# Kernel tuning notes

Measured on AMD Instinct MI355X. Metric: run time of the kernel, lower is better.

The kernel has to match this reference:

```python
import jax, jax.numpy as jnp
import numpy as np

ENC_H = 512      # encoder_hidden_dim -> encoder_out feature = 2*ENC_H
DEC_H = 512      # decoder_hidden_dim
B, S = 32, 2048  # batch, max_seq_len


def setup_inputs() -> dict:
    key = jax.random.key(0)
    k1, k2, k3, k4, k5, k6, k7 = jax.random.split(key, 7)
    encoder_out = jax.random.normal(k1, (B, S, 2 * ENC_H), dtype=jnp.float32)
    hidden = jax.random.normal(k2, (B, DEC_H), dtype=jnp.float32)
    lengths = jax.random.randint(k3, (B,), 1, S + 1, dtype=jnp.int64)
    in_dim = 2 * ENC_H + DEC_H
    # torch nn.Linear default init scale
    attn_w = jax.random.uniform(k4, (DEC_H, in_dim), jnp.float32, -1.0, 1.0) / np.sqrt(in_dim)
    attn_b = jax.random.uniform(k5, (DEC_H,), jnp.float32, -1.0, 1.0) / np.sqrt(in_dim)
    v_w = jax.random.uniform(k6, (1, DEC_H), jnp.float32, -1.0, 1.0) / np.sqrt(DEC_H)
    v_b = jax.random.uniform(k7, (1,), jnp.float32, -1.0, 1.0) / np.sqrt(DEC_H)
    return {"encoder_out": encoder_out, "hidden": hidden, "lengths": lengths,
            "attn_w": attn_w, "attn_b": attn_b, "v_w": v_w, "v_b": v_b}


def reference(encoder_out, hidden, lengths, attn_w, attn_b, v_w, v_b):
    # encoder_out: [B,S,2E], hidden: [B,D], lengths: [B]
    Bc, Sc, _ = encoder_out.shape
    h = jnp.broadcast_to(hidden[:, None, :], (Bc, Sc, hidden.shape[-1]))
    temp = jnp.concatenate([h, encoder_out], axis=2)           # [B,S,D+2E]
    e = jnp.tanh(jnp.einsum('bsf,df->bsd', temp, attn_w) + attn_b)  # [B,S,D]
    scores = jnp.einsum('bsd,d->bs', e, v_w[0]) + v_b[0]       # [B,S]
    mask = jnp.arange(Sc)[None, :] < lengths[:, None]          # [B,S]
    scores = jnp.where(mask, scores, -jnp.inf)
    energy = jax.nn.softmax(scores, axis=1)                    # softmax over valid positions
    energy = jnp.where(mask, energy, 0.0)                      # padded positions stay exactly 0
    context = jnp.einsum('bs,bse->be', energy, encoder_out)    # [B,2E]
    return context
```

## Files before the change

### kernel.cpp

```cpp
#include <hip/hip_runtime.h>
#include <hip/hip_bf16.h>
#include <math.h>

typedef __attribute__((ext_vector_type(4))) short short4v;
typedef __attribute__((ext_vector_type(8))) short short8;
typedef __attribute__((ext_vector_type(16))) float f32x16;

static constexpr int B  = 32;
static constexpr int S  = 2048;
static constexpr int D  = 512;
static constexpr int KE = 1024;
static constexpr int IN = 1536;

__device__ __forceinline__ unsigned pk2(float lo, float hi) {
    __hip_bfloat162 t = __float22bfloat162_rn(make_float2(lo, hi));
    unsigned u;
    __builtin_memcpy(&u, &t, 4);
    return u;
}

__device__ __forceinline__ short4v pack4(float4 f) {
    unsigned u2[2] = { pk2(f.x, f.y), pk2(f.z, f.w) };
    short4v r;
    __builtin_memcpy(&r, u2, 8);
    return r;
}

__device__ __forceinline__ short8 pack8(float4 f0, float4 f1) {
    unsigned u[4] = { pk2(f0.x, f0.y), pk2(f0.z, f0.w), pk2(f1.x, f1.y), pk2(f1.z, f1.w) };
    short8 r;
    __builtin_memcpy(&r, u, 16);
    return r;
}

__device__ __forceinline__ short8 cat44(short4v lo, short4v hi) {
    short8 r;
    __builtin_memcpy(&r, &lo, 8);
    __builtin_memcpy(((char*)&r) + 8, &hi, 8);
    return r;
}

__device__ __forceinline__ float tanh_fast(float x) {
    float e = __expf(2.0f * x);
    return (e - 1.0f) * __builtin_amdgcn_rcpf(e + 1.0f);
}

__global__ void k_prep(const float* __restrict__ attn_w,
                       const float* __restrict__ hidden,
                       const float* __restrict__ attn_b,
                       unsigned short* __restrict__ Bf,
                       float* __restrict__ u) {
    if (blockIdx.x < 256) {
        int o = blockIdx.x * 256 + threadIdx.x;
        int l6  = o & 63;
        int grp = o >> 6;
        int d = (grp & 15) * 32 + (l6 & 31);
        int k = (grp >> 4) * 16 + (l6 >> 5) * 8;
        const float* src = attn_w + (size_t)d * IN + 512 + k;
        float4 f0 = *(const float4*)src;
        float4 f1 = *(const float4*)(src + 4);
        ((short8*)Bf)[o] = pack8(f0, f1);
    } else {
        int gid = (blockIdx.x - 256) * 256 + threadIdx.x;
        int b = gid >> 9;
        int d = gid & (D - 1);
        const float* h = hidden + b * D;
        const float* w = attn_w + (size_t)d * IN;
        float acc = attn_b[d];
        for (int k = 0; k < D; k += 4) {
            float4 hv = *(const float4*)(h + k);
            float4 wv = *(const float4*)(w + k);
            acc += hv.x * wv.x + hv.y * wv.y + hv.z * wv.z + hv.w * wv.w;
        }
        u[gid] = acc;
    }
}

#define LOADB(K, DST) do {                                     \
    _Pragma("unroll")                                          \
    for (int _jt = 0; _jt < 4; _jt++)                          \
        DST[_jt] = bb[(size_t)(K) * 1024 + _jt * 64];          \
} while (0)

__global__ __launch_bounds__(256, 3) void k_fused(
    const float* __restrict__ enc, const unsigned short* __restrict__ Bfrag,
    const float* __restrict__ u, const float* __restrict__ v_w,
    const float* __restrict__ v_b, const int* __restrict__ lengths,
    float* __restrict__ num, float* __restrict__ den)
{
    __shared__ short4v ldsA[2][32 * 19];
    __shared__ float sPart[4][32];
    __shared__ float sExp[32];

    const int b   = blockIdx.y;
    const int s0  = blockIdx.x * 32;
    const int len = lengths[b];
    if (s0 >= len) return;

    const int tid = threadIdx.x;
    const int w   = tid >> 6;
    const int l   = tid & 63;

    const float* encb = enc + ((size_t)b * S + s0) * KE;
    const int mr = tid >> 4;
    const int cw = tid & 15;
    const float* aG = encb + (size_t)mr * KE + cw * 4;
    const int wbase = mr * 19 + cw;

    const short8* bb = (const short8*)Bfrag + (w * 4) * 64 + l;

    f32x16 acc[4];
    #pragma unroll
    for (int jt = 0; jt < 4; jt++)
        #pragma unroll
        for (int e = 0; e < 16; e++) acc[jt][e] = 0.f;

    short8 pb[2][4];
    LOADB(0, pb[0]);
    LOADB(1, pb[1]);

    {
        float4 g0 = *(const float4*)aG;
        float4 g1 = *(const float4*)(aG + (size_t)16 * KE);
        ldsA[0][wbase]           = pack4(g0);
        ldsA[0][wbase + 16 * 19] = pack4(g1);
    }
    __syncthreads();

    const int rb0 = (l & 31) * 19 + (l >> 5) * 2;

    #pragma unroll 1
    for (int c = 0; c < 16; ++c) {
        const int buf = c & 1;
        const int cn  = (c + 1) & 15;
        float4 g0 = *(const float4*)(aG + cn * 64);
        float4 g1 = *(const float4*)(aG + (size_t)16 * KE + cn * 64);
        #pragma unroll
        for (int t2 = 0; t2 < 4; ++t2) {
            const short4v* base = &ldsA[buf][t2 * 4];
            short8 a0 = cat44(base[rb0], base[rb0 + 1]);
            const int bp = t2 & 1;
            #pragma unroll
            for (int jt = 0; jt < 4; jt++)
                acc[jt] = __builtin_amdgcn_mfma_f32_32x32x16_bf16(a0, pb[bp][jt], acc[jt], 0, 0, 0);
            LOADB((c * 4 + t2 + 2) & 63, pb[bp]);
        }
        __syncthreads();
        ldsA[buf ^ 1][wbase]           = pack4(g0);
        ldsA[buf ^ 1][wbase + 16 * 19] = pack4(g1);
        __syncthreads();
    }

    float vv[4], uu[4];
    const float* ub = u + b * D;
    #pragma unroll
    for (int jt = 0; jt < 4; jt++) {
        int d = w * 128 + jt * 32 + (l & 31);
        vv[jt] = v_w[d];
        uu[jt] = ub[d];
    }
    float red[16];
    #pragma unroll
    for (int r = 0; r < 16; r++) {
        float s = 0.f;
        #pragma unroll
        for (int jt = 0; jt < 4; jt++)
            s += vv[jt] * tanh_fast(acc[jt][r] + uu[jt]);
        red[r] = s;
    }
    #pragma unroll
    for (int off = 16; off >= 1; off >>= 1)
        #pragma unroll
        for (int r = 0; r < 16; r++)
            red[r] += __shfl_xor(red[r], off);
    if ((l & 31) == 0) {
        int hb = (l >> 5) * 4;
        #pragma unroll
        for (int r = 0; r < 16; r++)
            sPart[w][(r & 3) + 8 * (r >> 2) + hb] = red[r];
    }
    __syncthreads();

    if (tid < 32) {
        float sc = sPart[0][tid] + sPart[1][tid] + sPart[2][tid] + sPart[3][tid] + v_b[0];
        float wexp = (s0 + tid < len) ? __expf(sc) : 0.f;
        sExp[tid] = wexp;
        float dsum = wexp;
        #pragma unroll
        for (int off = 16; off >= 1; off >>= 1) dsum += __shfl_xor(dsum, off);
        if (tid == 0) atomicAdd(den + b, dsum);
    }
    __syncthreads();

    const float4* e4 = (const float4*)encb;
    float4 cacc[4];
    #pragma unroll
    for (int j = 0; j < 4; j++) cacc[j] = make_float4(0.f, 0.f, 0.f, 0.f);
    #pragma unroll
    for (int i = 0; i < 8; i++) {
        #pragma unroll
        for (int j = 0; j < 4; j++) {
            float wgt = sExp[i * 4 + j];
            float4 v = e4[(size_t)(i * 4 + j) * 256 + tid];
            cacc[j].x += wgt * v.x; cacc[j].y += wgt * v.y;
            cacc[j].z += wgt * v.z; cacc[j].w += wgt * v.w;
        }
    }
    #pragma unroll
    for (int j = 1; j < 4; j++) {
        cacc[0].x += cacc[j].x; cacc[0].y += cacc[j].y;
        cacc[0].z += cacc[j].z; cacc[0].w += cacc[j].w;
    }
    float* o = num + b * KE + tid * 4;
    atomicAdd(o + 0, cacc[0].x);
    atomicAdd(o + 1, cacc[0].y);
    atomicAdd(o + 2, cacc[0].z);
    atomicAdd(o + 3, cacc[0].w);
}

__global__ void k_norm(const float* __restrict__ num, const float* __restrict__ den,
                       float* __restrict__ out) {
    int b = blockIdx.x;
    int t = threadIdx.x;
    float inv = 1.f / den[b];
    float4 v = ((const float4*)(num + b * KE))[t];
    v.x *= inv; v.y *= inv; v.z *= inv; v.w *= inv;
    ((float4*)(out + b * KE))[t] = v;
}

extern "C" void kernel_launch(void* const* d_in, const int* in_sizes, int n_in,
                              void* d_out, int out_size, void* d_ws, size_t ws_size,
                              hipStream_t stream) {
    const float* enc    = (const float*)d_in[0];
    const float* hidden = (const float*)d_in[1];
    const int*   lengths= (const int*)d_in[2];
    const float* attn_w = (const float*)d_in[3];
    const float* attn_b = (const float*)d_in[4];
    const float* v_w    = (const float*)d_in[5];
    const float* v_b    = (const float*)d_in[6];
    float* out = (float*)d_out;

    float* ws  = (float*)d_ws;
    float* u   = ws;
    float* num = u + B * D;
    float* den = num + B * KE;
    unsigned short* Bf = (unsigned short*)(den + 32);

    (void)hipMemsetAsync(num, 0, (size_t)(B * KE + B) * sizeof(float), stream);
    k_prep <<<dim3(320), 256, 0, stream>>>(attn_w, hidden, attn_b, Bf, u);
    k_fused<<<dim3(S / 32, B), 256, 0, stream>>>(enc, Bf, u, v_w, v_b, lengths, num, den);
    k_norm <<<dim3(B), 256, 0, stream>>>(num, den, out);
}
```

Measured before the change: 451.8 us.

## Double M-tile per block to 64 rows, reusing B fragments across two MFMA tiles

Each block now handles 64 sequence positions instead of 32, with two 32-row accumulator sets that share each loaded B fragment, halving B-fragment traffic per row. The A-tile staging loop is restructured to a single sync per chunk, storing the next chunk before computing the current one, with four prefetched float4 loads per thread. Launch bounds drop to 2 blocks/SM to make room for the doubled accumulators. The costs are lower occupancy, coarser masking granularity (more wasted work past the sequence length), and fewer blocks overall.

```diff
diff --git a/kernel.cpp b/kernel.cpp
--- a/kernel.cpp
+++ b/kernel.cpp
@@ -82,18 +82,18 @@
         DST[_jt] = bb[(size_t)(K) * 1024 + _jt * 64];          \
 } while (0)
 
-__global__ __launch_bounds__(256, 3) void k_fused(
+__global__ __launch_bounds__(256, 2) void k_fused(
     const float* __restrict__ enc, const unsigned short* __restrict__ Bfrag,
     const float* __restrict__ u, const float* __restrict__ v_w,
     const float* __restrict__ v_b, const int* __restrict__ lengths,
     float* __restrict__ num, float* __restrict__ den)
 {
-    __shared__ short4v ldsA[2][32 * 19];
-    __shared__ float sPart[4][32];
-    __shared__ float sExp[32];
+    __shared__ short4v ldsA[2][64 * 19];
+    __shared__ float sPart[4][64];
+    __shared__ float sExp[64];
 
     const int b   = blockIdx.y;
-    const int s0  = blockIdx.x * 32;
+    const int s0  = blockIdx.x * 64;
     const int len = lengths[b];
     if (s0 >= len) return;
 
@@ -109,46 +109,54 @@
 
     const short8* bb = (const short8*)Bfrag + (w * 4) * 64 + l;
 
-    f32x16 acc[4];
-    #pragma unroll
-    for (int jt = 0; jt < 4; jt++)
-        #pragma unroll
-        for (int e = 0; e < 16; e++) acc[jt][e] = 0.f;
+    f32x16 acc[2][4];
+    #pragma unroll
+    for (int mt = 0; mt < 2; mt++)
+        #pragma unroll
+        for (int jt = 0; jt < 4; jt++)
+            #pragma unroll
+            for (int e = 0; e < 16; e++) acc[mt][jt][e] = 0.f;
 
     short8 pb[2][4];
     LOADB(0, pb[0]);
     LOADB(1, pb[1]);
 
-    {
-        float4 g0 = *(const float4*)aG;
-        float4 g1 = *(const float4*)(aG + (size_t)16 * KE);
-        ldsA[0][wbase]           = pack4(g0);
-        ldsA[0][wbase + 16 * 19] = pack4(g1);
-    }
-    __syncthreads();
+    float4 g[4];
+    #pragma unroll
+    for (int i = 0; i < 4; i++) g[i] = *(const float4*)(aG + (size_t)i * 16 * KE);
 
     const int rb0 = (l & 31) * 19 + (l >> 5) * 2;
+    const int rb1 = rb0 + 32 * 19;
 
     #pragma unroll 1
-    for (int c = 0; c < 16; ++c) {
-        const int buf = c & 1;
-        const int cn  = (c + 1) & 15;
-        float4 g0 = *(const float4*)(aG + cn * 64);
-        float4 g1 = *(const float4*)(aG + (size_t)16 * KE + cn * 64);
-        #pragma unroll
-        for (int t2 = 0; t2 < 4; ++t2) {
-            const short4v* base = &ldsA[buf][t2 * 4];
-            short8 a0 = cat44(base[rb0], base[rb0 + 1]);
-            const int bp = t2 & 1;
-            #pragma unroll
-            for (int jt = 0; jt < 4; jt++)
-                acc[jt] = __builtin_amdgcn_mfma_f32_32x32x16_bf16(a0, pb[bp][jt], acc[jt], 0, 0, 0);
-            LOADB((c * 4 + t2 + 2) & 63, pb[bp]);
-        }
+    for (int c = 0; c <= 16; ++c) {
         __syncthreads();
-        ldsA[buf ^ 1][wbase]           = pack4(g0);
-        ldsA[buf ^ 1][wbase + 16 * 19] = pack4(g1);
-        __syncthreads();
+        if (c < 16) {
+            #pragma unroll
+            for (int i = 0; i < 4; i++)
+                ldsA[c & 1][wbase + i * 16 * 19] = pack4(g[i]);
+            if (c < 15) {
+                #pragma unroll
+                for (int i = 0; i < 4; i++)
+                    g[i] = *(const float4*)(aG + (size_t)i * 16 * KE + (c + 1) * 64);
+            }
+        }
+        if (c > 0) {
+            const int buf = (c - 1) & 1;
+            #pragma unroll
+            for (int t2 = 0; t2 < 4; ++t2) {
+                const short4v* base = &ldsA[buf][t2 * 4];
+                short8 a0 = cat44(base[rb0], base[rb0 + 1]);
+                short8 a1 = cat44(base[rb1], base[rb1 + 1]);
+                const int bp = t2 & 1;
+                #pragma unroll
+                for (int jt = 0; jt < 4; jt++) {
+                    acc[0][jt] = __builtin_amdgcn_mfma_f32_32x32x16_bf16(a0, pb[bp][jt], acc[0][jt], 0, 0, 0);
+                    acc[1][jt] = __builtin_amdgcn_mfma_f32_32x32x16_bf16(a1, pb[bp][jt], acc[1][jt], 0, 0, 0);
+                }
+                LOADB(((c - 1) * 4 + t2 + 2) & 63, pb[bp]);
+            }
+        }
     }
 
     float vv[4], uu[4];
@@ -159,36 +167,41 @@
         vv[jt] = v_w[d];
         uu[jt] = ub[d];
     }
-    float red[16];
-    #pragma unroll
-    for (int r = 0; r < 16; r++) {
-        float s = 0.f;
-        #pragma unroll
-        for (int jt = 0; jt < 4; jt++)
-            s += vv[jt] * tanh_fast(acc[jt][r] + uu[jt]);
-        red[r] = s;
-    }
+    float red[2][16];
+    #pragma unroll
+    for (int mt = 0; mt < 2; mt++)
+        #pragma unroll
+        for (int r = 0; r < 16; r++) {
+            float s = 0.f;
+            #pragma unroll
+            for (int jt = 0; jt < 4; jt++)
+                s += vv[jt] * tanh_fast(acc[mt][jt][r] + uu[jt]);
+            red[mt][r] = s;
+        }
     #pragma unroll
     for (int off = 16; off >= 1; off >>= 1)
         #pragma unroll
-        for (int r = 0; r < 16; r++)
-            red[r] += __shfl_xor(red[r], off);
+        for (int mt = 0; mt < 2; mt++)
+            #pragma unroll
+            for (int r = 0; r < 16; r++)
+                red[mt][r] += __shfl_xor(red[mt][r], off);
     if ((l & 31) == 0) {
         int hb = (l >> 5) * 4;
         #pragma unroll
-        for (int r = 0; r < 16; r++)
-            sPart[w][(r & 3) + 8 * (r >> 2) + hb] = red[r];
+        for (int mt = 0; mt < 2; mt++)
+            #pragma unroll
+            for (int r = 0; r < 16; r++)
+                sPart[w][mt * 32 + (r & 3) + 8 * (r >> 2) + hb] = red[mt][r];
     }
     __syncthreads();
 
-    if (tid < 32) {
+    if (tid < 64) {
         float sc = sPart[0][tid] + sPart[1][tid] + sPart[2][tid] + sPart[3][tid] + v_b[0];
         float wexp = (s0 + tid < len) ? __expf(sc) : 0.f;
         sExp[tid] = wexp;
-        float dsum = wexp;
-        #pragma unroll
-        for (int off = 16; off >= 1; off >>= 1) dsum += __shfl_xor(dsum, off);
-        if (tid == 0) atomicAdd(den + b, dsum);
+        #pragma unroll
+        for (int off = 32; off >= 1; off >>= 1) wexp += __shfl_xor(wexp, off);
+        if (tid == 0) atomicAdd(den + b, wexp);
     }
     __syncthreads();
 
@@ -197,7 +210,7 @@
     #pragma unroll
     for (int j = 0; j < 4; j++) cacc[j] = make_float4(0.f, 0.f, 0.f, 0.f);
     #pragma unroll
-    for (int i = 0; i < 8; i++) {
+    for (int i = 0; i < 16; i++) {
         #pragma unroll
         for (int j = 0; j < 4; j++) {
             float wgt = sExp[i * 4 + j];
@@ -248,6 +261,6 @@
 
     (void)hipMemsetAsync(num, 0, (size_t)(B * KE + B) * sizeof(float), stream);
     k_prep <<<dim3(320), 256, 0, stream>>>(attn_w, hidden, attn_b, Bf, u);
-    k_fused<<<dim3(S / 32, B), 256, 0, stream>>>(enc, Bf, u, v_w, v_b, lengths, num, den);
+    k_fused<<<dim3(S / 64, B), 256, 0, stream>>>(enc, Bf, u, v_w, v_b, lengths, num, den);
     k_norm <<<dim3(B), 256, 0, stream>>>(num, den, out);
 }
```

New measurement: 437.9 us. -3.1%, faster.
